# Optimization experiments

Measured on AMD Instinct MI355X. Metric: run time of the kernel, lower is better.

The kernel has to match this reference:

```python
import jax, jax.numpy as jnp
import numpy as np

N = 20000   # nodes
E = 400000  # edges per hop
IN_C = 256
HID = 128
HEADS = 2
OUT_C = 256
RELU_SLOPE = 0.2  # GATConv LeakyReLU negative slope
EPS = 1e-16


def _segment_mean(vals, idx, num_segments):
    s = jax.ops.segment_sum(vals, idx, num_segments=num_segments)
    cnt = jax.ops.segment_sum(jnp.ones((vals.shape[0], 1), vals.dtype), idx,
                              num_segments=num_segments)
    return s / (cnt + EPS)


def _gat(x, src, dst, Wg, a_src, a_dst, bg):
    # x: [N, IN_C] -> h: [N, HEADS, HID]
    h = (x @ Wg).reshape(N, HEADS, HID)
    alpha_s = jnp.sum(h * a_src, axis=-1)  # [N, HEADS]
    alpha_d = jnp.sum(h * a_dst, axis=-1)  # [N, HEADS]
    logits = jax.nn.leaky_relu(alpha_s[src] + alpha_d[dst], RELU_SLOPE)  # [E, HEADS]
    # softmax over incoming edges per destination node
    m = jax.ops.segment_max(logits, dst, num_segments=N)  # [N, HEADS]
    m = jnp.where(jnp.isfinite(m), m, 0.0)
    ex = jnp.exp(logits - m[dst])
    denom = jax.ops.segment_sum(ex, dst, num_segments=N)  # [N, HEADS]
    alpha = ex / (denom[dst] + EPS)  # [E, HEADS]
    msg = h[src] * alpha[..., None]  # [E, HEADS, HID]
    out = jax.ops.segment_sum(msg, dst, num_segments=N)  # [N, HEADS, HID]
    return out.reshape(N, HEADS * HID) + bg


def setup_inputs() -> dict:
    key = jax.random.key(0)
    ks = jax.random.split(key, 16)

    def xav(k, shape):
        fan_in, fan_out = shape[0], shape[-1]
        lim = np.sqrt(6.0 / (fan_in + fan_out)).astype(np.float32)
        return jax.random.uniform(k, shape, jnp.float32, -lim, lim)

    inp = {
        "x": jax.random.normal(ks[0], (N, IN_C), jnp.float32),
        "edge_index_1hop": jax.random.randint(ks[1], (2, E), 0, N),
        "edge_time_1hop": jax.random.uniform(ks[2], (E,), jnp.float32),
        "edge_index_2hop": jax.random.randint(ks[3], (2, E), 0, N),
        "edge_time_2hop": jax.random.uniform(ks[4], (E,), jnp.float32),
        "rel_embeddings": jax.random.normal(ks[5], (N, HID), jnp.float32),
        # GATConv params
        "Wg": xav(ks[6], (IN_C, HEADS * HID)),
        "a_src": jax.random.normal(ks[7], (HEADS, HID), jnp.float32) * 0.1,
        "a_dst": jax.random.normal(ks[8], (HEADS, HID), jnp.float32) * 0.1,
        "bg": jnp.zeros((HEADS * HID,), jnp.float32),
        # linear_transform
        "W_lin": xav(ks[9], (HEADS * HID, OUT_C)),
        "b_lin": jnp.zeros((OUT_C,), jnp.float32),
        # time_gate: in = 2*(OUT_C+1)
        "W_tg": xav(ks[10], (2 * (OUT_C + 1), 1)),
        "b_tg": jnp.zeros((1,), jnp.float32),
        # semantic_gate: in = (OUT_C+1) + HID + 1
        "W_sg": xav(ks[11], (OUT_C + 1 + HID + 1, 1)),
        "b_sg": jnp.zeros((1,), jnp.float32),
    }
    return inp


def reference(x, edge_index_1hop, edge_time_1hop, edge_index_2hop,
              edge_time_2hop, rel_embeddings, Wg, a_src, a_dst, bg,
              W_lin, b_lin, W_tg, b_tg, W_sg, b_sg):
    src1, dst1 = edge_index_1hop[0], edge_index_1hop[1]
    src2, dst2 = edge_index_2hop[0], edge_index_2hop[1]

    # ---- 1-hop aggregation ----
    x_1hop = _gat(x, src1, dst1, Wg, a_src, a_dst, bg) @ W_lin + b_lin  # [N, OUT_C]
    time_e1 = edge_time_1hop[:, None]  # [E, 1]
    node_time = _segment_mean(time_e1, dst1, N)  # [N, 1]
    x_1hop_t = jnp.concatenate([x_1hop, node_time], axis=-1)  # [N, OUT_C+1]

    # ---- semantic gate (per 1-hop edge -> per node) ----
    combined = jnp.concatenate(
        [x_1hop_t[src1], rel_embeddings[dst1], time_e1], axis=-1)  # [E, OUT_C+1+HID+1]
    sem_w_edge = jax.nn.sigmoid(combined @ W_sg + b_sg)  # [E, 1]
    sem_w_node = _segment_mean(sem_w_edge, dst1, N)  # [N, 1]

    # ---- 2-hop aggregation, semantically weighted ----
    x_2hop = _gat(x, src2, dst2, Wg, a_src, a_dst, bg) @ W_lin + b_lin  # [N, OUT_C]
    x_2hop = x_2hop * sem_w_node
    x_2hop_t = jnp.concatenate([x_2hop, node_time], axis=-1)  # [N, OUT_C+1]

    # ---- time-gated fusion ----
    gate_in = jnp.concatenate([x_1hop_t, x_2hop_t], axis=-1)  # [N, 2*(OUT_C+1)]
    g = jax.nn.sigmoid(gate_in @ W_tg + b_tg)  # [N, 1]
    return g * x_2hop_t + (1.0 - g) * x_1hop_t
```

## Files before the change

kernel.cpp:

```cpp
#include <hip/hip_runtime.h>
#include <math.h>

constexpr float EPSF = 1e-16f;
#define MAXDEG 64
#define BINCH 4096
#define NBUCK 64

typedef __attribute__((ext_vector_type(8))) short bfrag;
typedef __attribute__((ext_vector_type(4))) float ffrag;

__device__ __forceinline__ float leaky(float v){ return v >= 0.f ? v : 0.2f*v; }

__device__ __forceinline__ ushort f2bf(float f){
  union { float f; unsigned u; } v; v.f = f;
  unsigned r = (v.u + 0x7FFFu + ((v.u >> 16) & 1u)) >> 16;
  return (ushort)r;
}
__device__ __forceinline__ float bf2f(ushort u){
  union { unsigned u; float f; } v; v.u = ((unsigned)u) << 16;
  return v.f;
}

__device__ __forceinline__ float wred_max(float v){
  #pragma unroll
  for (int d = 32; d; d >>= 1) v = fmaxf(v, __shfl_xor(v, d));
  return v;
}
__device__ __forceinline__ float wred_sum(float v){
  #pragma unroll
  for (int d = 32; d; d >>= 1) v += __shfl_xor(v, d);
  return v;
}


__global__ __launch_bounds__(256) void k_prep(const float* __restrict__ Wg, const float* __restrict__ Wlin,
    const float* __restrict__ rel, const float* __restrict__ Wsg,
    ushort* __restrict__ Wgt, ushort* __restrict__ Wlt, float* __restrict__ p2, int N){
  __shared__ float tile[32][33];
  int b = blockIdx.x, t = threadIdx.x;
  if (b < 128){
    const float* W = (b < 64) ? Wg : Wlin;
    ushort* Wt = (b < 64) ? Wgt : Wlt;
    int bb = b & 63;
    int bx = (bb & 7)*32, by = (bb >> 3)*32;
    int tx = t & 31, ty = t >> 5;
    for (int r = ty; r < 32; r += 8) tile[r][tx] = W[(size_t)(by+r)*256 + bx+tx];
    __syncthreads();
    for (int r = ty; r < 32; r += 8) Wt[(size_t)(bx+r)*256 + by+tx] = f2bf(tile[tx][r]);
  } else {
    int node = (b-128)*4 + (t>>6);
    if (node >= N) return;
    int lane = t & 63;
    const float* rr = rel + (size_t)node*128;
    float q = rr[lane]*Wsg[257+lane] + rr[64+lane]*Wsg[321+lane];
    q = wred_sum(q);
    if (lane == 0) p2[node] = q;
  }
}


__global__ __launch_bounds__(256) void k_work1(const float* __restrict__ x, const ushort* __restrict__ Wgt,
    const float* __restrict__ a_src, const float* __restrict__ a_dst,
    ushort* __restrict__ hb, float* __restrict__ as_, float* __restrict__ ad_,
    const int* __restrict__ ei1, const float* __restrict__ et1, const int* __restrict__ ei2,
    int* __restrict__ gcur, int2* __restrict__ bkt1, int2* __restrict__ bkt2,
    int cap1, int cap2, int N, int E1, int E2, int GB1, int B1, int NB){
  __shared__ int hist[NBUCK];
  __shared__ int loff[NBUCK+1];
  __shared__ int cur[NBUCK];
  __shared__ int gbase_s[NBUCK];
  __shared__ int2 stage[BINCH];
  int bid = blockIdx.x, t = threadIdx.x;
  if (bid >= GB1){
    int hop = (bid >= GB1 + B1);
    int cb  = hop ? (bid - GB1 - B1) : (bid - GB1);
    const int* src_arr = hop ? ei2 : ei1;
    const int* dst_arr = hop ? (ei2 + E2) : (ei1 + E1);
    int Eh = hop ? E2 : E1;
    int c0 = cb * BINCH;
    int M = Eh - c0; if (M > BINCH) M = BINCH;
    if (t < NBUCK) hist[t] = 0;
    __syncthreads();
    #pragma unroll
    for (int k = 0; k < BINCH/256; k++){
      int i = k*256 + t;
      if (i < M) atomicAdd(&hist[dst_arr[c0 + i] / NB], 1);
    }
    __syncthreads();
    if (t < NBUCK){
      int v = hist[t];
      int xx = v;
      #pragma unroll
      for (int d = 1; d < NBUCK; d <<= 1){
        int y = __shfl_up(xx, d);
        if (t >= d) xx += y;
      }
      loff[t+1] = xx;
      if (t == 0) loff[0] = 0;
      cur[t] = xx - v;
      gbase_s[t] = atomicAdd(&gcur[hop*NBUCK + t], v);
    }
    __syncthreads();
    #pragma unroll
    for (int k = 0; k < BINCH/256; k++){
      int i = k*256 + t;
      if (i < M){
        int s = src_arr[c0 + i];
        int d = dst_arr[c0 + i];
        int b = d / NB;
        int ld = d - b*NB;
        int pos = atomicAdd(&cur[b], 1);
        float tv = hop ? 0.f : et1[c0 + i];
        stage[pos] = make_int2(s | (ld << 15), __float_as_int(tv));
      }
    }
    __syncthreads();
    int2* bkt = hop ? bkt2 : bkt1;
    int cap = hop ? cap2 : cap1;
    for (int s = t; s < M; s += 256){
      int lo = 0, hi = NBUCK;
      while (hi - lo > 1){ int mid = (lo + hi) >> 1; if (loff[mid] <= s) lo = mid; else hi = mid; }
      int gpos = gbase_s[lo] + (s - loff[lo]);
      if (gpos < cap) bkt[(size_t)lo*cap + gpos] = stage[s];
    }
    return;
  }
  int head = bid & 1;
  int bx = bid >> 1;
  int wid = t >> 6, lane = t & 63;
  int wr = wid >> 1, wc = wid & 1;
  int row0 = bx*128 + wr*64;
  int col0 = head*128 + wc*64;
  int l15 = lane & 15, lk = lane >> 4;
  ffrag acc[4][4];
  #pragma unroll
  for (int i = 0; i < 4; i++)
    #pragma unroll
    for (int j = 0; j < 4; j++){ ffrag z; z[0]=0.f; z[1]=0.f; z[2]=0.f; z[3]=0.f; acc[i][j] = z; }
  for (int kk = 0; kk < 256; kk += 32){
    bfrag a[4], b[4];
    #pragma unroll
    for (int i = 0; i < 4; i++){
      int r = row0 + i*16 + l15; if (r > N-1) r = N-1;
      float4 u0 = *(const float4*)(x + (size_t)r*256 + kk + lk*8);
      float4 u1 = *(const float4*)(x + (size_t)r*256 + kk + lk*8 + 4);
      bfrag tv;
      tv[0]=(short)f2bf(u0.x); tv[1]=(short)f2bf(u0.y); tv[2]=(short)f2bf(u0.z); tv[3]=(short)f2bf(u0.w);
      tv[4]=(short)f2bf(u1.x); tv[5]=(short)f2bf(u1.y); tv[6]=(short)f2bf(u1.z); tv[7]=(short)f2bf(u1.w);
      a[i] = tv;
      int c = col0 + i*16 + l15;
      b[i] = *(const bfrag*)(Wgt + (size_t)c*256 + kk + lk*8);
    }
    #pragma unroll
    for (int i = 0; i < 4; i++)
      #pragma unroll
      for (int j = 0; j < 4; j++)
        acc[i][j] = __builtin_amdgcn_mfma_f32_16x16x32_bf16(a[i], b[j], acc[i][j], 0, 0, 0);
  }
  float asv[4], adv[4];
  #pragma unroll
  for (int j = 0; j < 4; j++){
    int cc = wc*64 + j*16 + l15;
    asv[j] = a_src[head*128 + cc];
    adv[j] = a_dst[head*128 + cc];
  }
  #pragma unroll
  for (int i = 0; i < 4; i++){
    float ps[4] = {0.f,0.f,0.f,0.f}, pd[4] = {0.f,0.f,0.f,0.f};
    #pragma unroll
    for (int j = 0; j < 4; j++){
      int c = col0 + j*16 + l15;
      #pragma unroll
      for (int q = 0; q < 4; q++){
        int r = row0 + i*16 + lk*4 + q;
        float v = acc[i][j][q];
        if (r < N) hb[(size_t)r*256 + c] = f2bf(v);
        ps[q] = fmaf(v, asv[j], ps[q]);
        pd[q] = fmaf(v, adv[j], pd[q]);
      }
    }
    #pragma unroll
    for (int q = 0; q < 4; q++){
      #pragma unroll
      for (int d = 1; d < 16; d <<= 1){
        ps[q] += __shfl_xor(ps[q], d);
        pd[q] += __shfl_xor(pd[q], d);
      }
      int r = row0 + i*16 + lk*4 + q;
      if (l15 == 0 && r < N){
        atomicAdd(&as_[r*2 + head], ps[q]);
        atomicAdd(&ad_[r*2 + head], pd[q]);
      }
    }
  }
}


__global__ __launch_bounds__(256) void k_place(const int* __restrict__ gcur,
    const int2* __restrict__ bkt1, const int2* __restrict__ bkt2, int cap1, int cap2,
    int* __restrict__ ssrc1, int* __restrict__ ssrc2, float* __restrict__ stime1,
    int* __restrict__ cntg, float* __restrict__ ntime, float* __restrict__ p1,
    const float* __restrict__ Wsg, int N, int NB){
  __shared__ int   cnt_l[512];
  __shared__ float ts_l[512];
  int b = blockIdx.x & 63, hop = blockIdx.x >> 6;
  int t = threadIdx.x;
  int nbase = b * NB;
  int ncnt = N - nbase; if (ncnt > NB) ncnt = NB; if (ncnt < 0) ncnt = 0;
  for (int i = t; i < NB; i += 256){ cnt_l[i] = 0; ts_l[i] = 0.f; }
  __syncthreads();
  const int2* bkt = hop ? bkt2 : bkt1;
  int cap = hop ? cap2 : cap1;
  int len = gcur[hop*NBUCK + b]; if (len > cap) len = cap;
  int* ssrc = hop ? ssrc2 : ssrc1;
  for (int i = t; i < len; i += 256){
    int2 en = bkt[(size_t)b*cap + i];
    int src = en.x & 0x7FFF;
    int ld  = en.x >> 15;
    int slot = atomicAdd(&cnt_l[ld], 1);
    if (slot < MAXDEG){
      size_t o = (size_t)(nbase + ld)*MAXDEG + slot;
      ssrc[o] = src;
      if (hop == 0) stime1[o] = __int_as_float(en.y);
    }
    if (hop == 0) atomicAdd(&ts_l[ld], __int_as_float(en.y));
  }
  __syncthreads();
  float w256 = Wsg[256];
  for (int ld = t; ld < ncnt; ld += 256){
    int node = nbase + ld;
    int c = cnt_l[ld];
    cntg[hop*N + node] = c;
    if (hop == 0){
      float nt = ts_l[ld] / ((float)c + EPSF);
      ntime[node] = nt;
      p1[node] = nt * w256;
    }
  }
}


__global__ __launch_bounds__(256) void k_node(const int* __restrict__ cntg,
    const int* __restrict__ ssrc1, const int* __restrict__ ssrc2,
    const float* __restrict__ as_, const float* __restrict__ ad_,
    const ushort* __restrict__ h, const float* __restrict__ bg,
    ushort* __restrict__ gatb, int N, int gN4){
  __shared__ float2 s_ew[4][MAXDEG];
  __shared__ int    s_src[4][MAXDEG];
  int wid = threadIdx.x >> 6, lane = threadIdx.x & 63;
  int hop = blockIdx.x >= gN4;
  int node = (blockIdx.x - (hop ? gN4 : 0))*4 + wid;
  bool active = node < N;
  const int* ssrc = hop ? ssrc2 : ssrc1;
  int deg = 0; float ad0 = 0.f, ad1 = 0.f;
  if (active){
    int degt = cntg[hop*N + node];
    deg = degt > MAXDEG ? MAXDEG : degt;
    ad0 = ad_[node*2]; ad1 = ad_[node*2+1];
  }
  size_t o0 = (size_t)node * MAXDEG;
  float m0 = -INFINITY, m1 = -INFINITY;
  for (int i = lane; i < deg; i += 64){
    int s = ssrc[o0 + i];
    s_src[wid][i] = s;
    float2 a = ((const float2*)as_)[s];
    float l0 = leaky(a.x + ad0), l1 = leaky(a.y + ad1);
    s_ew[wid][i] = make_float2(l0, l1);
    m0 = fmaxf(m0, l0); m1 = fmaxf(m1, l1);
  }
  m0 = wred_max(m0); m1 = wred_max(m1);
  if (deg == 0){ m0 = 0.f; m1 = 0.f; }
  float e0 = 0.f, e1 = 0.f;
  for (int i = lane; i < deg; i += 64){
    float2 l = s_ew[wid][i];
    float x0 = __expf(l.x - m0), x1 = __expf(l.y - m1);
    s_ew[wid][i] = make_float2(x0, x1);
    e0 += x0; e1 += x1;
  }
  e0 = wred_sum(e0); e1 = wred_sum(e1);
  __syncthreads();
  if (!active) return;
  int head = lane >> 5, c0 = lane << 2;
  float rd = 1.f / ((head ? e1 : e0) + EPSF);
  float ax=0.f, ay=0.f, az=0.f, aw=0.f;
  float bx=0.f, by=0.f, bz=0.f, bw=0.f;
  int i = 0;
  for (; i + 2 <= deg; i += 2){
    int s0 = s_src[wid][i], s1 = s_src[wid][i+1];
    float2 w0 = s_ew[wid][i], w1 = s_ew[wid][i+1];
    float f0 = head ? w0.y : w0.x;
    float f1 = head ? w1.y : w1.x;
    ushort4 u0 = *(const ushort4*)(h + (size_t)s0*256 + c0);
    ushort4 u1 = *(const ushort4*)(h + (size_t)s1*256 + c0);
    ax = fmaf(f0, bf2f(u0.x), ax); ay = fmaf(f0, bf2f(u0.y), ay);
    az = fmaf(f0, bf2f(u0.z), az); aw = fmaf(f0, bf2f(u0.w), aw);
    bx = fmaf(f1, bf2f(u1.x), bx); by = fmaf(f1, bf2f(u1.y), by);
    bz = fmaf(f1, bf2f(u1.z), bz); bw = fmaf(f1, bf2f(u1.w), bw);
  }
  if (i < deg){
    int s0 = s_src[wid][i];
    float2 w0 = s_ew[wid][i];
    float f0 = head ? w0.y : w0.x;
    ushort4 u0 = *(const ushort4*)(h + (size_t)s0*256 + c0);
    ax = fmaf(f0, bf2f(u0.x), ax); ay = fmaf(f0, bf2f(u0.y), ay);
    az = fmaf(f0, bf2f(u0.z), az); aw = fmaf(f0, bf2f(u0.w), aw);
  }
  float4 bgv = *(const float4*)(bg + c0);
  ushort4 o;
  o.x = f2bf((ax+bx)*rd + bgv.x); o.y = f2bf((ay+by)*rd + bgv.y);
  o.z = f2bf((az+bz)*rd + bgv.z); o.w = f2bf((aw+bw)*rd + bgv.w);
  *(ushort4*)(gatb + (size_t)(hop ? N + node : node)*256 + c0) = o;
}


__global__ __launch_bounds__(256) void k_gemm2(const ushort* __restrict__ A, const ushort* __restrict__ Bt,
    const float* __restrict__ bias, const float* __restrict__ Wsg,
    float* __restrict__ Cf, float* __restrict__ p1, int M, int N){
  int wid = threadIdx.x >> 6, lane = threadIdx.x & 63;
  int wr = wid >> 1, wc = wid & 1;
  int row0 = blockIdx.x*128 + wr*64;
  int col0 = blockIdx.y*128 + wc*64;
  int l15 = lane & 15, lk = lane >> 4;
  ffrag acc[4][4];
  #pragma unroll
  for (int i = 0; i < 4; i++)
    #pragma unroll
    for (int j = 0; j < 4; j++){ ffrag z; z[0]=0.f; z[1]=0.f; z[2]=0.f; z[3]=0.f; acc[i][j] = z; }
  for (int kk = 0; kk < 256; kk += 32){
    bfrag a[4], b[4];
    #pragma unroll
    for (int i = 0; i < 4; i++){
      int r = row0 + i*16 + l15; if (r > M-1) r = M-1;
      a[i] = *(const bfrag*)(A + (size_t)r*256 + kk + lk*8);
      int c = col0 + i*16 + l15;
      b[i] = *(const bfrag*)(Bt + (size_t)c*256 + kk + lk*8);
    }
    #pragma unroll
    for (int i = 0; i < 4; i++)
      #pragma unroll
      for (int j = 0; j < 4; j++)
        acc[i][j] = __builtin_amdgcn_mfma_f32_16x16x32_bf16(a[i], b[j], acc[i][j], 0, 0, 0);
  }
  float wsv[4]; float bv[4];
  #pragma unroll
  for (int j = 0; j < 4; j++){
    int c = col0 + j*16 + l15;
    wsv[j] = Wsg[c];
    bv[j] = bias[c];
  }
  #pragma unroll
  for (int i = 0; i < 4; i++){
    float ps[4] = {0.f,0.f,0.f,0.f};
    #pragma unroll
    for (int j = 0; j < 4; j++){
      int c = col0 + j*16 + l15;
      #pragma unroll
      for (int q = 0; q < 4; q++){
        int r = row0 + i*16 + lk*4 + q;
        float v = acc[i][j][q] + bv[j];
        if (r < M) Cf[(size_t)r*256 + c] = v;
        ps[q] = fmaf(v, wsv[j], ps[q]);
      }
    }
    #pragma unroll
    for (int q = 0; q < 4; q++){
      #pragma unroll
      for (int d = 1; d < 16; d <<= 1) ps[q] += __shfl_xor(ps[q], d);
      int r = row0 + i*16 + lk*4 + q;
      if (l15 == 0 && r < N) atomicAdd(&p1[r], ps[q]);
    }
  }
}


__global__ __launch_bounds__(256) void k_final(const float* __restrict__ x1, const float* __restrict__ x2r,
    const int* __restrict__ cntg, const int* __restrict__ ssrc1, const float* __restrict__ stime1,
    const float* __restrict__ p1, const float* __restrict__ p2,
    const float* __restrict__ Wsg, const float* __restrict__ bsg,
    const float* __restrict__ ntime, const float* __restrict__ Wtg, const float* __restrict__ btg,
    float* __restrict__ out, int N){
  int node = blockIdx.x*4 + (threadIdx.x>>6);
  if (node >= N) return;
  int lane = threadIdx.x & 63;
  int degt = cntg[node];
  int deg = degt > MAXDEG ? MAXDEG : degt;
  float acc = 0.f;
  if (lane < deg){
    size_t o = (size_t)node*MAXDEG + lane;
    float z = p1[ssrc1[o]] + p2[node] + bsg[0] + stime1[o]*Wsg[385];
    acc = 1.f / (1.f + __expf(-z));
  }
  acc = wred_sum(acc);
  float sm = acc / ((float)degt + EPSF);
  float nt = ntime[node];
  int c0 = lane << 2;
  float4 a4 = *(const float4*)(x1  + (size_t)node*256 + c0);
  float4 r4 = *(const float4*)(x2r + (size_t)node*256 + c0);
  float4 b4; b4.x = r4.x*sm; b4.y = r4.y*sm; b4.z = r4.z*sm; b4.w = r4.w*sm;
  float4 w1 = *(const float4*)(Wtg + c0);
  float4 w2 = *(const float4*)(Wtg + 257 + c0);
  float s = a4.x*w1.x + a4.y*w1.y + a4.z*w1.z + a4.w*w1.w
          + b4.x*w2.x + b4.y*w2.y + b4.z*w2.z + b4.w*w2.w;
  if (lane == 0) s += nt*Wtg[256] + nt*Wtg[513] + btg[0];
  s = wred_sum(s);
  float g = 1.f / (1.f + __expf(-s));
  float* orow = out + (size_t)node*257;
  orow[c0+0] = g*b4.x + (1.f - g)*a4.x;
  orow[c0+1] = g*b4.y + (1.f - g)*a4.y;
  orow[c0+2] = g*b4.z + (1.f - g)*a4.z;
  orow[c0+3] = g*b4.w + (1.f - g)*a4.w;
  if (lane == 0) orow[256] = nt;
}


extern "C" void kernel_launch(void* const* d_in, const int* in_sizes, int n_in,
                              void* d_out, int out_size, void* d_ws, size_t ws_size,
                              hipStream_t stream){
  const float* x    = (const float*)d_in[0];
  const int*   ei1  = (const int*)d_in[1];
  const float* et1  = (const float*)d_in[2];
  const int*   ei2  = (const int*)d_in[3];
  const float* rel  = (const float*)d_in[5];
  const float* Wg   = (const float*)d_in[6];
  const float* asrc = (const float*)d_in[7];
  const float* adst = (const float*)d_in[8];
  const float* bg   = (const float*)d_in[9];
  const float* Wlin = (const float*)d_in[10];
  const float* blin = (const float*)d_in[11];
  const float* Wtg  = (const float*)d_in[12];
  const float* btg  = (const float*)d_in[13];
  const float* Wsg  = (const float*)d_in[14];
  const float* bsg  = (const float*)d_in[15];
  float* out = (float*)d_out;

  const int N  = in_sizes[0] / 256;
  const int E1 = in_sizes[1] / 2;
  const int E2 = in_sizes[3] / 2;
  const int NB = (N + NBUCK - 1) / NBUCK;
  const int cap1 = E1/NBUCK + 2048;
  const int cap2 = E2/NBUCK + 2048;

  char* base = (char*)d_ws;
  size_t off = 0;
  auto alloc = [&](size_t bytes)->char*{
    char* p = base + off;
    off += (bytes + 255) & ~(size_t)255;
    return p;
  };
  int*    gcur  = (int*)alloc((size_t)2*NBUCK*4);
  float*  as_   = (float*)alloc((size_t)2*N*4);
  float*  ad_   = (float*)alloc((size_t)2*N*4);
  size_t zero_bytes = off;
  ushort* Wgt   = (ushort*)alloc((size_t)256*256*2);
  ushort* Wlt   = (ushort*)alloc((size_t)256*256*2);
  ushort* hb    = (ushort*)alloc((size_t)N*256*2);
  ushort* gatb  = (ushort*)alloc((size_t)2*N*256*2);
  float*  x12   = (float*)alloc((size_t)2*N*256*4);
  float*  ntime = (float*)alloc((size_t)N*4);
  float*  p1    = (float*)alloc((size_t)N*4);
  float*  p2    = (float*)alloc((size_t)N*4);
  int*    cntg  = (int*)alloc((size_t)2*N*4);
  int*    ssrc1 = (int*)alloc((size_t)N*MAXDEG*4);
  int*    ssrc2 = (int*)alloc((size_t)N*MAXDEG*4);
  float*  stime1= (float*)alloc((size_t)N*MAXDEG*4);
  int2*   bkt1  = (int2*)alloc((size_t)NBUCK*cap1*8);
  int2*   bkt2  = (int2*)alloc((size_t)NBUCK*cap2*8);

  dim3 blk(256);
  int gN4 = (N + 3) / 4;
  int GB1 = ((N + 127) / 128) * 2;
  int B1  = (E1 + BINCH - 1) / BINCH;
  int B2  = (E2 + BINCH - 1) / BINCH;
  dim3 ggemm2((2*N + 127) / 128, 2);

  hipMemsetAsync(d_ws, 0, zero_bytes, stream);
  k_prep<<<128 + gN4, blk, 0, stream>>>(Wg, Wlin, rel, Wsg, Wgt, Wlt, p2, N);
  k_work1<<<GB1 + B1 + B2, blk, 0, stream>>>(x, Wgt, asrc, adst, hb, as_, ad_,
                                             ei1, et1, ei2, gcur, bkt1, bkt2,
                                             cap1, cap2, N, E1, E2, GB1, B1, NB);
  k_place<<<128, blk, 0, stream>>>(gcur, bkt1, bkt2, cap1, cap2, ssrc1, ssrc2, stime1,
                                   cntg, ntime, p1, Wsg, N, NB);
  k_node<<<2*gN4, blk, 0, stream>>>(cntg, ssrc1, ssrc2, as_, ad_, hb, bg, gatb, N, gN4);
  k_gemm2<<<ggemm2, blk, 0, stream>>>(gatb, Wlt, blin, Wsg, x12, p1, 2*N, N);
  k_final<<<gN4, blk, 0, stream>>>(x12, x12 + (size_t)N*256, cntg, ssrc1, stime1,
                                   p1, p2, Wsg, bsg, ntime, Wtg, btg, out, N);
}
```

Baseline: 160.8 us.

## Restructure GAT node aggregation with register softmax and 16-byte split-edge gathers

The per-node softmax now keeps each edge's logit in a register (one edge per lane, since degree is capped at 64). This removes the two shared-memory loops and the block-wide __syncthreads. The aggregation loop now splits the wave into two half-waves that each process alternate edges with 16-byte bf16 loads of 8 channels. The halves are combined with a cross-half shuffle, and the weights are pre-normalised. The aim is wider memory transactions, more loads in flight per wave and less synchronisation. The cost is an extra shuffle reduction and half the lanes idling during the store.

```diff
diff --git a/kernel.cpp b/kernel.cpp
--- a/kernel.cpp
+++ b/kernel.cpp
@@ -8,6 +8,7 @@
 
 typedef __attribute__((ext_vector_type(8))) short bfrag;
 typedef __attribute__((ext_vector_type(4))) float ffrag;
+typedef __attribute__((ext_vector_type(8))) unsigned short ushortv8;
 
 __device__ __forceinline__ float leaky(float v){ return v >= 0.f ? v : 0.2f*v; }
 
@@ -245,8 +246,8 @@
     const float* __restrict__ as_, const float* __restrict__ ad_,
     const ushort* __restrict__ h, const float* __restrict__ bg,
     ushort* __restrict__ gatb, int N, int gN4){
-  __shared__ float2 s_ew[4][MAXDEG];
-  __shared__ int    s_src[4][MAXDEG];
+  __shared__ int   s_src[4][MAXDEG];
+  __shared__ float2 s_w[4][MAXDEG];
   int wid = threadIdx.x >> 6, lane = threadIdx.x & 63;
   int hop = blockIdx.x >= gN4;
   int node = (blockIdx.x - (hop ? gN4 : 0))*4 + wid;
@@ -259,57 +260,59 @@
     ad0 = ad_[node*2]; ad1 = ad_[node*2+1];
   }
   size_t o0 = (size_t)node * MAXDEG;
-  float m0 = -INFINITY, m1 = -INFINITY;
-  for (int i = lane; i < deg; i += 64){
-    int s = ssrc[o0 + i];
-    s_src[wid][i] = s;
-    float2 a = ((const float2*)as_)[s];
-    float l0 = leaky(a.x + ad0), l1 = leaky(a.y + ad1);
-    s_ew[wid][i] = make_float2(l0, l1);
-    m0 = fmaxf(m0, l0); m1 = fmaxf(m1, l1);
-  }
-  m0 = wred_max(m0); m1 = wred_max(m1);
-  if (deg == 0){ m0 = 0.f; m1 = 0.f; }
-  float e0 = 0.f, e1 = 0.f;
-  for (int i = lane; i < deg; i += 64){
-    float2 l = s_ew[wid][i];
-    float x0 = __expf(l.x - m0), x1 = __expf(l.y - m1);
-    s_ew[wid][i] = make_float2(x0, x1);
-    e0 += x0; e1 += x1;
-  }
-  e0 = wred_sum(e0); e1 = wred_sum(e1);
-  __syncthreads();
+  int msrc = 0;
+  float l0 = -INFINITY, l1 = -INFINITY;
+  if (lane < deg){
+    msrc = ssrc[o0 + lane];
+    float2 a = ((const float2*)as_)[msrc];
+    l0 = leaky(a.x + ad0); l1 = leaky(a.y + ad1);
+  }
+  float m0 = wred_max(l0), m1 = wred_max(l1);
+  float x0 = 0.f, x1 = 0.f;
+  if (lane < deg){ x0 = __expf(l0 - m0); x1 = __expf(l1 - m1); }
+  float e0 = wred_sum(x0), e1 = wred_sum(x1);
+  float rd0 = 1.f/(e0 + EPSF), rd1 = 1.f/(e1 + EPSF);
+  s_src[wid][lane] = msrc;
+  s_w[wid][lane] = make_float2(x0*rd0, x1*rd1);
   if (!active) return;
-  int head = lane >> 5, c0 = lane << 2;
-  float rd = 1.f / ((head ? e1 : e0) + EPSF);
-  float ax=0.f, ay=0.f, az=0.f, aw=0.f;
-  float bx=0.f, by=0.f, bz=0.f, bw=0.f;
+  int eh = lane >> 5, cl = lane & 31, ch0 = cl << 3, head = cl >> 4;
+  float acc[8] = {0.f,0.f,0.f,0.f,0.f,0.f,0.f,0.f};
   int i = 0;
-  for (; i + 2 <= deg; i += 2){
-    int s0 = s_src[wid][i], s1 = s_src[wid][i+1];
-    float2 w0 = s_ew[wid][i], w1 = s_ew[wid][i+1];
-    float f0 = head ? w0.y : w0.x;
-    float f1 = head ? w1.y : w1.x;
-    ushort4 u0 = *(const ushort4*)(h + (size_t)s0*256 + c0);
-    ushort4 u1 = *(const ushort4*)(h + (size_t)s1*256 + c0);
-    ax = fmaf(f0, bf2f(u0.x), ax); ay = fmaf(f0, bf2f(u0.y), ay);
-    az = fmaf(f0, bf2f(u0.z), az); aw = fmaf(f0, bf2f(u0.w), aw);
-    bx = fmaf(f1, bf2f(u1.x), bx); by = fmaf(f1, bf2f(u1.y), by);
-    bz = fmaf(f1, bf2f(u1.z), bz); bw = fmaf(f1, bf2f(u1.w), bw);
-  }
-  if (i < deg){
-    int s0 = s_src[wid][i];
-    float2 w0 = s_ew[wid][i];
-    float f0 = head ? w0.y : w0.x;
-    ushort4 u0 = *(const ushort4*)(h + (size_t)s0*256 + c0);
-    ax = fmaf(f0, bf2f(u0.x), ax); ay = fmaf(f0, bf2f(u0.y), ay);
-    az = fmaf(f0, bf2f(u0.z), az); aw = fmaf(f0, bf2f(u0.w), aw);
-  }
-  float4 bgv = *(const float4*)(bg + c0);
-  ushort4 o;
-  o.x = f2bf((ax+bx)*rd + bgv.x); o.y = f2bf((ay+by)*rd + bgv.y);
-  o.z = f2bf((az+bz)*rd + bgv.z); o.w = f2bf((aw+bw)*rd + bgv.w);
-  *(ushort4*)(gatb + (size_t)(hop ? N + node : node)*256 + c0) = o;
+  for (; i + 4 <= deg; i += 4){
+    int eA = i + eh, eB = i + 2 + eh;
+    int sA = s_src[wid][eA], sB = s_src[wid][eB];
+    float2 wA2 = s_w[wid][eA], wB2 = s_w[wid][eB];
+    float wA = head ? wA2.y : wA2.x;
+    float wB = head ? wB2.y : wB2.x;
+    ushortv8 uA = *(const ushortv8*)(h + (size_t)sA*256 + ch0);
+    ushortv8 uB = *(const ushortv8*)(h + (size_t)sB*256 + ch0);
+    #pragma unroll
+    for (int k = 0; k < 8; k++) acc[k] = fmaf(wA, bf2f(uA[k]), acc[k]);
+    #pragma unroll
+    for (int k = 0; k < 8; k++) acc[k] = fmaf(wB, bf2f(uB[k]), acc[k]);
+  }
+  for (; i < deg; i += 2){
+    int e = i + eh;
+    bool v = e < deg;
+    int s = v ? s_src[wid][e] : 0;
+    float w = 0.f;
+    if (v){ float2 w2 = s_w[wid][e]; w = head ? w2.y : w2.x; }
+    ushortv8 u = *(const ushortv8*)(h + (size_t)s*256 + ch0);
+    #pragma unroll
+    for (int k = 0; k < 8; k++) acc[k] = fmaf(w, bf2f(u[k]), acc[k]);
+  }
+  #pragma unroll
+  for (int k = 0; k < 8; k++) acc[k] += __shfl_xor(acc[k], 32);
+  if (eh == 0){
+    float4 b0 = *(const float4*)(bg + ch0);
+    float4 b1 = *(const float4*)(bg + ch0 + 4);
+    ushortv8 o;
+    o[0] = f2bf(acc[0] + b0.x); o[1] = f2bf(acc[1] + b0.y);
+    o[2] = f2bf(acc[2] + b0.z); o[3] = f2bf(acc[3] + b0.w);
+    o[4] = f2bf(acc[4] + b1.x); o[5] = f2bf(acc[5] + b1.y);
+    o[6] = f2bf(acc[6] + b1.z); o[7] = f2bf(acc[7] + b1.w);
+    *(ushortv8*)(gatb + (size_t)(hop ? N + node : node)*256 + ch0) = o;
+  }
 }
 
 
```

Result: no change. 158.1 us (-1.7%).
